# Kernel optimization log

Measured on AMD Instinct MI355X. Metric: run time of the kernel, lower is better.

The kernel has to match this reference:

```python
import jax, jax.numpy as jnp
import numpy as np

BLOCK_SIZE = 1024
OUTLIER_SIGMA = 3.0
OUT_FEATURES = 11008
IN_FEATURES = 4096
TOKENS = 64


def _quantize_mixed_np(W):
    """Faithful numpy port of quantize_mixed (BLOCK_SIZE divides numel exactly here)."""
    flat = W.astype(np.float32).reshape(-1)
    nb = flat.size // BLOCK_SIZE
    blocks = flat.reshape(nb, BLOCK_SIZE)
    mu = blocks.mean(axis=1, keepdims=True)
    sig = np.maximum(blocks.std(axis=1, ddof=1, keepdims=True), 1e-8)  # torch.std is unbiased
    outlier = np.abs(blocks - mu) > OUTLIER_SIGMA * sig
    abs_max = np.maximum(np.abs(np.where(outlier, 0.0, blocks)).max(axis=1), 1e-8)
    scales = (abs_max / 127.0).astype(np.float16)
    q = np.clip(np.round(blocks / abs_max[:, None] * 127.0), -127, 127).astype(np.int8)
    all_pos = np.arange(nb, dtype=np.int64)[:, None] * BLOCK_SIZE + np.arange(BLOCK_SIZE, dtype=np.int64)[None, :]
    int8_data = q[~outlier]                      # row-major == torch order
    fp16_data = blocks[outlier].astype(np.float16)
    int8_pos = all_pos[~outlier].astype(np.int32)
    fp16_pos = all_pos[outlier].astype(np.int32)
    block_idx = np.nonzero(~outlier)[0].astype(np.int32)  # block index per int8 value
    return int8_data, fp16_data, scales, int8_pos, fp16_pos, block_idx


def setup_inputs() -> dict:
    key = jax.random.key(0)
    k_x, k_b = jax.random.split(key)
    rng = np.random.default_rng(0)
    W = (rng.standard_normal((OUT_FEATURES, IN_FEATURES)) * 0.02).astype(np.float32)
    int8_data, fp16_data, scales, int8_pos, fp16_pos, block_idx = _quantize_mixed_np(W)
    x = jax.random.normal(k_x, (TOKENS, IN_FEATURES), dtype=jnp.float16)
    bias = jax.random.normal(k_b, (OUT_FEATURES,), dtype=jnp.float16) * jnp.float16(0.02)
    return {
        "x": x,
        "int8_data": jnp.asarray(int8_data),
        "fp16_data": jnp.asarray(fp16_data),
        "scales": jnp.asarray(scales),
        "bias": bias,
        "int8_pos": jnp.asarray(int8_pos),
        "fp16_pos": jnp.asarray(fp16_pos),
        "block_idx": jnp.asarray(block_idx),
    }


def reference(x, int8_data, fp16_data, scales, bias, int8_pos, fp16_pos, block_idx):
    out_features = bias.shape[0]
    in_features = x.shape[1]
    numel = out_features * in_features  # divisible by BLOCK_SIZE for these dims
    # dequantize_mixed: scatter fp16 outliers and dequantized int8 values into flat fp16 buffer
    flat = jnp.zeros((numel,), dtype=jnp.float16)
    flat = flat.at[fp16_pos].set(fp16_data)
    flat = flat.at[int8_pos].set(int8_data.astype(jnp.float16) * scales[block_idx])
    W = flat.reshape(out_features, in_features)
    # F.linear(x, W, bias) in fp16
    return jnp.dot(x.astype(jnp.float16), W.T) + bias
```

## Files before the change

### kernel.cpp

```cpp
#include <hip/hip_runtime.h>
#include <hip/hip_fp16.h>

#define TOK   64
#define INF   4096
#define OUTF  11008
#define NUMEL (OUTF * INF)
#define NSLC  (NUMEL / 64)
#define NBLK  (OUTF / 16)
#define NCH   8

typedef __attribute__((ext_vector_type(8))) _Float16 half8;
typedef __attribute__((ext_vector_type(4))) _Float16 half4;
typedef __attribute__((ext_vector_type(4))) float floatx4;
typedef __attribute__((ext_vector_type(4), aligned(4))) int int4u;
typedef __attribute__((ext_vector_type(4))) int int4a;

#define BPAD 520

__global__ __launch_bounds__(256) void precompute_kernel(
    const float* __restrict__ x, const int* __restrict__ fppos, int nf,
    _Float16* __restrict__ x16, int* __restrict__ meta) {
  const int t = blockIdx.x * 256 + threadIdx.x;
  if (t < (TOK * INF) / 4) {
    const floatx4 f = *(const floatx4*)&x[t * 4];
    half4 h;
    h[0] = (_Float16)f[0]; h[1] = (_Float16)f[1];
    h[2] = (_Float16)f[2]; h[3] = (_Float16)f[3];
    *(half4*)&x16[t * 4] = h;
  }
  if (t < NSLC) {
    const int target = t << 6;
    int lo = 0, hi = nf;
    while (lo < hi) {
      const int mid = (lo + hi) >> 1;
      if (fppos[mid] < target) lo = mid + 1; else hi = mid;
    }
    unsigned long long mask = 0ull;
    int j = lo;
    while (j < nf) {
      const int d = fppos[j] - target;
      if (d >= 64) break;
      mask |= 1ull << d;
      ++j;
    }
    int4a mv;
    mv[0] = lo;
    mv[1] = (int)(unsigned)(mask & 0xffffffffu);
    mv[2] = (int)(unsigned)(mask >> 32);
    mv[3] = 0;
    *(int4a*)&meta[t * 4] = mv;
  }
}

__device__ __forceinline__ void meta_window(const int p0, const int4a mv,
                                            int& i0, unsigned& m8) {
  const unsigned mlo = (unsigned)mv[1];
  const unsigned mhi = (unsigned)mv[2];
  const int off = p0 & 63;
  m8 = 0xffu & (off < 32 ? (mlo >> off) : (mhi >> (off - 32)));
  const unsigned bl = (off >= 32) ? mlo : (mlo & ((1u << off) - 1u));
  const unsigned bh = (off >= 32) ? (mhi & ((1u << (off - 32)) - 1u)) : 0u;
  i0 = p0 - mv[0] - (__popc(bl) + __popc(bh));
}

__device__ __forceinline__ half8 finish_slot(
    const unsigned m8, const int i0, const int p0, const float s,
    const int (&l)[8], const int* __restrict__ i8,
    const float* __restrict__ fpdat, const int n8) {
  const int f = (int)m8;
  float ov[8];
#pragma unroll
  for (int e = 0; e < 8; ++e) ov[e] = 0.f;
  if (f) {
    int fi = p0 - i0;
#pragma unroll
    for (int e = 0; e < 8; ++e) {
      if ((f >> e) & 1) { ov[e] = fpdat[fi]; ++fi; }
    }
  }

  half8 oh;
  if (i0 + 8 <= n8) {
    if (f == 0) {
#pragma unroll
      for (int e = 0; e < 8; ++e) oh[e] = (_Float16)((float)l[e] * s);
    } else {
      int q = 0;
#pragma unroll
      for (int e = 0; e < 8; ++e) {
        const int flg = (f >> e) & 1;
        int lv = l[0];
#pragma unroll
        for (int qq = 1; qq < 8; ++qq) lv = (q == qq) ? l[qq] : lv;
        oh[e] = flg ? (_Float16)ov[e] : (_Float16)((float)lv * s);
        q += 1 - flg;
      }
    }
  } else {
    int c = 0;
    const int m = n8 - 1;
#pragma unroll
    for (int e = 0; e < 8; ++e) {
      const int flg = (f >> e) & 1;
      int idx = i0 + e - c;
      idx = idx < 0 ? 0 : (idx > m ? m : idx);
      oh[e] = flg ? (_Float16)ov[e] : (_Float16)((float)i8[idx] * s);
      c += flg;
    }
  }
  return oh;
}

__global__ __launch_bounds__(256) void gemm_fused(
    const _Float16* __restrict__ x16, const int* __restrict__ i8,
    const float* __restrict__ fpdat, const float* __restrict__ scales,
    const int* __restrict__ meta, const float* __restrict__ bias,
    float* __restrict__ out, const int n8) {
  __shared__ __attribute__((aligned(16))) char smem[2 * 16 * BPAD * 2];
  _Float16 (* __restrict__ Bt)[16][BPAD] = (_Float16 (*)[16][BPAD])smem;
  float* red = (float*)smem;

  const int tid  = threadIdx.x;
  const int wave = tid >> 6;
  const int lane = tid & 63;
  const int quad = lane >> 4;
  const int ln   = lane & 15;
  const int n0   = blockIdx.x << 4;

  int rL[4], k8o[4];
#pragma unroll
  for (int i = 0; i < 4; ++i) {
    const int slot = i * 256 + tid;
    rL[i]  = slot >> 6;
    k8o[i] = (slot & 63) * 8;
  }

  int4a  mreg[2][4];
  float  sreg[2][4];
  int    lreg[4][8];
  int    i0v[4];
  unsigned m8v[4];

#pragma unroll
  for (int i = 0; i < 4; ++i) {
    const int p0 = (n0 + rL[i]) * INF + k8o[i];
    mreg[0][i] = *(const int4a*)&meta[(p0 >> 6) * 4];
    sreg[0][i] = scales[p0 >> 10];
  }
#pragma unroll
  for (int i = 0; i < 4; ++i) {
    const int p0 = (n0 + rL[i]) * INF + 512 + k8o[i];
    mreg[1][i] = *(const int4a*)&meta[(p0 >> 6) * 4];
    sreg[1][i] = scales[p0 >> 10];
  }
#pragma unroll
  for (int i = 0; i < 4; ++i) {
    const int p0 = (n0 + rL[i]) * INF + k8o[i];
    meta_window(p0, mreg[0][i], i0v[i], m8v[i]);
    if (i0v[i] + 8 <= n8) {
      *(int4u*)&lreg[i][0] = *(const int4u*)&i8[i0v[i]];
      *(int4u*)&lreg[i][4] = *(const int4u*)&i8[i0v[i] + 4];
    }
  }
#pragma unroll
  for (int i = 0; i < 4; ++i) {
    const int p0 = (n0 + rL[i]) * INF + k8o[i];
    const half8 oh = finish_slot(m8v[i], i0v[i], p0, sreg[0][i], lreg[i],
                                 i8, fpdat, n8);
    *(half8*)&Bt[0][rL[i]][k8o[i]] = oh;
  }
  __syncthreads();

  floatx4 acc0 = {0,0,0,0}, acc1 = {0,0,0,0}, acc2 = {0,0,0,0}, acc3 = {0,0,0,0};

#pragma unroll
  for (int c = 0; c < NCH; ++c) {
    const int cur = c & 1;

    if (c + 1 < NCH) {
      const int bk = (c + 1) & 1;
#pragma unroll
      for (int i = 0; i < 4; ++i) {
        const int p0 = (n0 + rL[i]) * INF + (c + 1) * 512 + k8o[i];
        meta_window(p0, mreg[bk][i], i0v[i], m8v[i]);
        if (i0v[i] + 8 <= n8) {
          *(int4u*)&lreg[i][0] = *(const int4u*)&i8[i0v[i]];
          *(int4u*)&lreg[i][4] = *(const int4u*)&i8[i0v[i] + 4];
        }
      }
      if (c + 2 < NCH) {
        const int bk2 = c & 1;
#pragma unroll
        for (int i = 0; i < 4; ++i) {
          const int p0 = (n0 + rL[i]) * INF + (c + 2) * 512 + k8o[i];
          mreg[bk2][i] = *(const int4a*)&meta[(p0 >> 6) * 4];
          sreg[bk2][i] = scales[p0 >> 10];
        }
      }
    }

    {
      const _Float16* ap = &x16[ln * INF + c * 512 + wave * 128 + quad * 8];
      const _Float16* bp = &Bt[cur][ln][wave * 128 + quad * 8];
#pragma unroll
      for (int st = 0; st < 4; ++st) {
        const int ko = st * 32;
        const half8 bh = *(const half8*)&bp[ko];
        const half8 a0 = *(const half8*)&ap[ko];
        const half8 a1 = *(const half8*)&ap[16 * INF + ko];
        const half8 a2 = *(const half8*)&ap[32 * INF + ko];
        const half8 a3 = *(const half8*)&ap[48 * INF + ko];
        acc0 = __builtin_amdgcn_mfma_f32_16x16x32_f16(a0, bh, acc0, 0, 0, 0);
        acc1 = __builtin_amdgcn_mfma_f32_16x16x32_f16(a1, bh, acc1, 0, 0, 0);
        acc2 = __builtin_amdgcn_mfma_f32_16x16x32_f16(a2, bh, acc2, 0, 0, 0);
        acc3 = __builtin_amdgcn_mfma_f32_16x16x32_f16(a3, bh, acc3, 0, 0, 0);
      }
    }

    if (c + 1 < NCH) {
      const int bk = (c + 1) & 1;
      half8 oh[4];
#pragma unroll
      for (int i = 0; i < 4; ++i) {
        const int p0 = (n0 + rL[i]) * INF + (c + 1) * 512 + k8o[i];
        oh[i] = finish_slot(m8v[i], i0v[i], p0, sreg[bk][i], lreg[i],
                            i8, fpdat, n8);
      }
#pragma unroll
      for (int i = 0; i < 4; ++i)
        *(half8*)&Bt[bk][rL[i]][k8o[i]] = oh[i];
      __syncthreads();
    }
  }

  const int mb = quad * 4;
#pragma unroll
  for (int i = 0; i < 4; ++i) red[wave * 1024 + (mb + i)      * 16 + ln] = acc0[i];
#pragma unroll
  for (int i = 0; i < 4; ++i) red[wave * 1024 + (16 + mb + i) * 16 + ln] = acc1[i];
#pragma unroll
  for (int i = 0; i < 4; ++i) red[wave * 1024 + (32 + mb + i) * 16 + ln] = acc2[i];
#pragma unroll
  for (int i = 0; i < 4; ++i) red[wave * 1024 + (48 + mb + i) * 16 + ln] = acc3[i];
  __syncthreads();

#pragma unroll
  for (int c2 = 0; c2 < 4; ++c2) {
    const int cell = tid + c2 * 256;
    const int mm = cell >> 4, nn = cell & 15;
    const float v = red[cell] + red[1024 + cell] + red[2048 + cell]
                  + red[3072 + cell] + bias[n0 + nn];
    out[mm * OUTF + n0 + nn] = v;
  }
}

extern "C" void kernel_launch(void* const* d_in, const int* in_sizes, int n_in,
                              void* d_out, int out_size, void* d_ws,
                              size_t ws_size, hipStream_t stream) {
  const float* x      = (const float*)d_in[0];
  const int*   i8     = (const int*)d_in[1];
  const float* fpdat  = (const float*)d_in[2];
  const float* scales = (const float*)d_in[3];
  const float* bias   = (const float*)d_in[4];
  const int*   fppos  = (const int*)d_in[6];

  char* wsp = (char*)d_ws;
  _Float16* x16  = (_Float16*)wsp;
  int*      meta = (int*)(wsp + (size_t)TOK * INF * sizeof(_Float16));
  float*    out  = (float*)d_out;

  const int n8 = in_sizes[1];
  const int nf = in_sizes[2];

  precompute_kernel<<<NSLC / 256, 256, 0, stream>>>(x, fppos, nf, x16, meta);
  gemm_fused<<<NBLK, 256, 0, stream>>>(x16, i8, fpdat, scales, meta, bias,
                                       out, n8);
}
```

Baseline: 539.6 us.

## Split K four ways in fused dequant GEMM with separate reduction kernel

```diff
diff --git a/kernel.cpp b/kernel.cpp
--- a/kernel.cpp
+++ b/kernel.cpp
@@ -7,7 +7,9 @@
 #define NUMEL (OUTF * INF)
 #define NSLC  (NUMEL / 64)
 #define NBLK  (OUTF / 16)
-#define NCH   8
+#define KSPL  4
+#define NCH   4
+#define OUTN  (TOK * OUTF)
 
 typedef __attribute__((ext_vector_type(8))) _Float16 half8;
 typedef __attribute__((ext_vector_type(4))) _Float16 half4;
@@ -15,7 +17,7 @@
 typedef __attribute__((ext_vector_type(4), aligned(4))) int int4u;
 typedef __attribute__((ext_vector_type(4))) int int4a;
 
-#define BPAD 520
+#define BPAD 264
 
 __global__ __launch_bounds__(256) void precompute_kernel(
     const float* __restrict__ x, const int* __restrict__ fppos, int nf,
@@ -111,11 +113,10 @@
   return oh;
 }
 
-__global__ __launch_bounds__(256) void gemm_fused(
+__global__ __launch_bounds__(256, 4) void gemm_fused(
     const _Float16* __restrict__ x16, const int* __restrict__ i8,
     const float* __restrict__ fpdat, const float* __restrict__ scales,
-    const int* __restrict__ meta, const float* __restrict__ bias,
-    float* __restrict__ out, const int n8) {
+    const int* __restrict__ meta, float* __restrict__ part, const int n8) {
   __shared__ __attribute__((aligned(16))) char smem[2 * 16 * BPAD * 2];
   _Float16 (* __restrict__ Bt)[16][BPAD] = (_Float16 (*)[16][BPAD])smem;
   float* red = (float*)smem;
@@ -125,37 +126,40 @@
   const int lane = tid & 63;
   const int quad = lane >> 4;
   const int ln   = lane & 15;
-  const int n0   = blockIdx.x << 4;
-
-  int rL[4], k8o[4];
-#pragma unroll
-  for (int i = 0; i < 4; ++i) {
+  const int nt   = blockIdx.x >> 2;
+  const int kq   = blockIdx.x & 3;
+  const int n0   = nt << 4;
+  const int kbas = kq * 1024;
+
+  int rL[2], k8o[2];
+#pragma unroll
+  for (int i = 0; i < 2; ++i) {
     const int slot = i * 256 + tid;
-    rL[i]  = slot >> 6;
-    k8o[i] = (slot & 63) * 8;
-  }
-
-  int4a  mreg[2][4];
-  float  sreg[2][4];
-  int    lreg[4][8];
-  int    i0v[4];
-  unsigned m8v[4];
-
-#pragma unroll
-  for (int i = 0; i < 4; ++i) {
-    const int p0 = (n0 + rL[i]) * INF + k8o[i];
+    rL[i]  = slot >> 5;
+    k8o[i] = (slot & 31) * 8;
+  }
+
+  int4a    mreg[2][2];
+  float    sreg[2][2];
+  int      lreg[2][8];
+  int      i0v[2];
+  unsigned m8v[2];
+
+#pragma unroll
+  for (int i = 0; i < 2; ++i) {
+    const int p0 = (n0 + rL[i]) * INF + kbas + k8o[i];
     mreg[0][i] = *(const int4a*)&meta[(p0 >> 6) * 4];
     sreg[0][i] = scales[p0 >> 10];
   }
 #pragma unroll
-  for (int i = 0; i < 4; ++i) {
-    const int p0 = (n0 + rL[i]) * INF + 512 + k8o[i];
+  for (int i = 0; i < 2; ++i) {
+    const int p0 = (n0 + rL[i]) * INF + kbas + 256 + k8o[i];
     mreg[1][i] = *(const int4a*)&meta[(p0 >> 6) * 4];
     sreg[1][i] = scales[p0 >> 10];
   }
 #pragma unroll
-  for (int i = 0; i < 4; ++i) {
-    const int p0 = (n0 + rL[i]) * INF + k8o[i];
+  for (int i = 0; i < 2; ++i) {
+    const int p0 = (n0 + rL[i]) * INF + kbas + k8o[i];
     meta_window(p0, mreg[0][i], i0v[i], m8v[i]);
     if (i0v[i] + 8 <= n8) {
       *(int4u*)&lreg[i][0] = *(const int4u*)&i8[i0v[i]];
@@ -163,8 +167,8 @@
     }
   }
 #pragma unroll
-  for (int i = 0; i < 4; ++i) {
-    const int p0 = (n0 + rL[i]) * INF + k8o[i];
+  for (int i = 0; i < 2; ++i) {
+    const int p0 = (n0 + rL[i]) * INF + kbas + k8o[i];
     const half8 oh = finish_slot(m8v[i], i0v[i], p0, sreg[0][i], lreg[i],
                                  i8, fpdat, n8);
     *(half8*)&Bt[0][rL[i]][k8o[i]] = oh;
@@ -180,8 +184,8 @@
     if (c + 1 < NCH) {
       const int bk = (c + 1) & 1;
 #pragma unroll
-      for (int i = 0; i < 4; ++i) {
-        const int p0 = (n0 + rL[i]) * INF + (c + 1) * 512 + k8o[i];
+      for (int i = 0; i < 2; ++i) {
+        const int p0 = (n0 + rL[i]) * INF + kbas + (c + 1) * 256 + k8o[i];
         meta_window(p0, mreg[bk][i], i0v[i], m8v[i]);
         if (i0v[i] + 8 <= n8) {
           *(int4u*)&lreg[i][0] = *(const int4u*)&i8[i0v[i]];
@@ -191,8 +195,8 @@
       if (c + 2 < NCH) {
         const int bk2 = c & 1;
 #pragma unroll
-        for (int i = 0; i < 4; ++i) {
-          const int p0 = (n0 + rL[i]) * INF + (c + 2) * 512 + k8o[i];
+        for (int i = 0; i < 2; ++i) {
+          const int p0 = (n0 + rL[i]) * INF + kbas + (c + 2) * 256 + k8o[i];
           mreg[bk2][i] = *(const int4a*)&meta[(p0 >> 6) * 4];
           sreg[bk2][i] = scales[p0 >> 10];
         }
@@ -200,10 +204,10 @@
     }
 
     {
-      const _Float16* ap = &x16[ln * INF + c * 512 + wave * 128 + quad * 8];
-      const _Float16* bp = &Bt[cur][ln][wave * 128 + quad * 8];
-#pragma unroll
-      for (int st = 0; st < 4; ++st) {
+      const _Float16* ap = &x16[ln * INF + kbas + c * 256 + wave * 64 + quad * 8];
+      const _Float16* bp = &Bt[cur][ln][wave * 64 + quad * 8];
+#pragma unroll
+      for (int st = 0; st < 2; ++st) {
         const int ko = st * 32;
         const half8 bh = *(const half8*)&bp[ko];
         const half8 a0 = *(const half8*)&ap[ko];
@@ -219,19 +223,20 @@
 
     if (c + 1 < NCH) {
       const int bk = (c + 1) & 1;
-      half8 oh[4];
-#pragma unroll
-      for (int i = 0; i < 4; ++i) {
-        const int p0 = (n0 + rL[i]) * INF + (c + 1) * 512 + k8o[i];
+      half8 oh[2];
+#pragma unroll
+      for (int i = 0; i < 2; ++i) {
+        const int p0 = (n0 + rL[i]) * INF + kbas + (c + 1) * 256 + k8o[i];
         oh[i] = finish_slot(m8v[i], i0v[i], p0, sreg[bk][i], lreg[i],
                             i8, fpdat, n8);
       }
 #pragma unroll
-      for (int i = 0; i < 4; ++i)
+      for (int i = 0; i < 2; ++i)
         *(half8*)&Bt[bk][rL[i]][k8o[i]] = oh[i];
       __syncthreads();
     }
   }
+  __syncthreads();
 
   const int mb = quad * 4;
 #pragma unroll
@@ -244,14 +249,31 @@
   for (int i = 0; i < 4; ++i) red[wave * 1024 + (48 + mb + i) * 16 + ln] = acc3[i];
   __syncthreads();
 
+  float* pp = &part[(size_t)kq * OUTN];
 #pragma unroll
   for (int c2 = 0; c2 < 4; ++c2) {
     const int cell = tid + c2 * 256;
     const int mm = cell >> 4, nn = cell & 15;
-    const float v = red[cell] + red[1024 + cell] + red[2048 + cell]
-                  + red[3072 + cell] + bias[n0 + nn];
-    out[mm * OUTF + n0 + nn] = v;
-  }
+    pp[mm * OUTF + n0 + nn] =
+        red[cell] + red[1024 + cell] + red[2048 + cell] + red[3072 + cell];
+  }
+}
+
+__global__ __launch_bounds__(256) void reduce_kernel(
+    const float* __restrict__ part, const float* __restrict__ bias,
+    float* __restrict__ out) {
+  const int t  = blockIdx.x * 256 + threadIdx.x;
+  const int i4 = t * 4;
+  floatx4 a = *(const floatx4*)&part[i4];
+#pragma unroll
+  for (int k = 1; k < KSPL; ++k) {
+    const floatx4 b = *(const floatx4*)&part[(size_t)k * OUTN + i4];
+    a[0] += b[0]; a[1] += b[1]; a[2] += b[2]; a[3] += b[3];
+  }
+  const int nn = i4 % OUTF;
+  const floatx4 bb = *(const floatx4*)&bias[nn];
+  a[0] += bb[0]; a[1] += bb[1]; a[2] += bb[2]; a[3] += bb[3];
+  *(floatx4*)&out[i4] = a;
 }
 
 extern "C" void kernel_launch(void* const* d_in, const int* in_sizes, int n_in,
@@ -267,12 +289,15 @@
   char* wsp = (char*)d_ws;
   _Float16* x16  = (_Float16*)wsp;
   int*      meta = (int*)(wsp + (size_t)TOK * INF * sizeof(_Float16));
+  float*    part = (float*)(wsp + (size_t)TOK * INF * sizeof(_Float16)
+                                + (size_t)NSLC * 16);
   float*    out  = (float*)d_out;
 
   const int n8 = in_sizes[1];
   const int nf = in_sizes[2];
 
   precompute_kernel<<<NSLC / 256, 256, 0, stream>>>(x, fppos, nf, x16, meta);
-  gemm_fused<<<NBLK, 256, 0, stream>>>(x16, i8, fpdat, scales, meta, bias,
-                                       out, n8);
-}
+  gemm_fused<<<NBLK * KSPL, 256, 0, stream>>>(x16, i8, fpdat, scales, meta,
+                                              part, n8);
+  reduce_kernel<<<OUTN / (4 * 256), 256, 0, stream>>>(part, bias, out);
+}
```

New measurement: 460.5 us. -14.7%, faster.
